# Optimization experiments

Hardware: AMD Instinct MI355X
Metric: run time of the kernel (lower is better)

## Reference

```python
import jax, jax.numpy as jnp
import numpy as np

OUT_H = 7  # _height_
OUT_W = 7  # _width_


def _bin_ids(start, end, size, nbins):
    # Per-pixel segment id along one spatial axis; id == nbins marks pixels outside the ROI.
    # Mirrors TF: step = int(region / nbins); bin i covers [i*step, (i+1)*step), last bin extends to region end.
    step = ((end - start).astype(jnp.float32) / nbins).astype(jnp.int32)
    idx = jnp.arange(size)
    rel = idx - start
    b = jnp.minimum(rel // jnp.maximum(step, 1), nbins - 1)
    b = jnp.where(step > 0, b, nbins - 1)  # degenerate step==0: everything valid falls in last bin
    valid = (rel >= 0) & (idx < end)
    return jnp.where(valid, b, nbins)


def _pool_one(fmap, roi):
    # fmap: [H, W, C], roi: [4] = (h_min, w_min, h_max, w_max) relative coords
    H, W, C = fmap.shape
    h0 = (H * roi[0]).astype(jnp.int32)
    w0 = (W * roi[1]).astype(jnp.int32)
    h1 = (H * roi[2]).astype(jnp.int32)
    w1 = (W * roi[3]).astype(jnp.int32)
    colb = _bin_ids(w0, w1, W, OUT_W)  # [W]
    rowb = _bin_ids(h0, h1, H, OUT_H)  # [H]
    # Max is separable over rows/cols: pool columns first, then rows.
    tmp = jax.ops.segment_max(jnp.transpose(fmap, (1, 0, 2)), colb, num_segments=OUT_W + 1)[:OUT_W]  # [OUT_W, H, C]
    out = jax.ops.segment_max(jnp.transpose(tmp, (1, 0, 2)), rowb, num_segments=OUT_H + 1)[:OUT_H]   # [OUT_H, OUT_W, C]
    return out


def _roi_pool(feature_map, rois):
    per_image = jax.vmap(_pool_one, in_axes=(None, 0))  # over ROIs
    return jax.vmap(per_image)(feature_map, rois)       # over batch -> [B, R, OUT_H, OUT_W, C]


def setup_inputs() -> dict:
    key = jax.random.key(0)
    k1, k2, k3 = jax.random.split(key, 3)
    B, H, W, C, R = 4, 56, 56, 256, 64
    feature_map = jax.random.normal(k1, (B, H, W, C), dtype=jnp.float32)
    # valid ROIs: (h_min, w_min) in [0, 0.45), extent in [0.30, 0.55) so every 7x7 bin is non-empty
    starts = jax.random.uniform(k2, (B, R, 2), minval=0.0, maxval=0.45, dtype=jnp.float32)
    lens = jax.random.uniform(k3, (B, R, 2), minval=0.30, maxval=0.55, dtype=jnp.float32)
    rois = jnp.concatenate([starts, jnp.minimum(starts + lens, 1.0)], axis=-1)  # [B, R, 4]
    return {"feature_map": feature_map, "rois": rois}


def reference(feature_map, rois):
    return _roi_pool(feature_map, rois)
```

## Files before the change

### kernel.cpp

```cpp
#include <hip/hip_runtime.h>


#define OUT_H 7
#define OUT_W 7
#define NBIN (OUT_H * OUT_W)
#define NB 4
#define NR 64
#define NH 56
#define NW 56
#define NC 256

#define BLKS_PER_XCD_SLOT 1568

typedef float v4f __attribute__((ext_vector_type(4)));

__global__ __launch_bounds__(64) void roi_pool_kernel(
    const float* __restrict__ fmap,
    const float* __restrict__ rois,
    float* __restrict__ out)
{
    const int blk  = blockIdx.x;
    const int xcd  = blk & 7;
    const int b    = xcd >> 1;
    const int work = ((xcd & 1) * BLKS_PER_XCD_SLOT) + (blk >> 3);
    const int r    = work / NBIN;
    const int bin  = work - r * NBIN;
    const int oi   = bin / OUT_W;
    const int oj   = bin - oi * OUT_W;

    const float* roi = rois + (size_t)(b * NR + r) * 4;
    const float r0 = roi[0], r1 = roi[1], r2 = roi[2], r3 = roi[3];
    const int h0 = (int)((float)NH * r0);
    const int w0 = (int)((float)NW * r1);
    const int h1 = (int)((float)NH * r2);
    const int w1 = (int)((float)NW * r3);

    const int hstep = (int)((float)(h1 - h0) / (float)OUT_H);
    const int wstep = (int)((float)(w1 - w0) / (float)OUT_W);

    int rlo, rhi, clo, chi;
    if (hstep >= 1) {
        rlo = h0 + oi * hstep;
        rhi = (oi < OUT_H - 1) ? (rlo + hstep) : h1;
    } else {
        rlo = (oi == OUT_H - 1) ? h0 : 0;
        rhi = (oi == OUT_H - 1) ? h1 : 0;
    }
    if (wstep >= 1) {
        clo = w0 + oj * wstep;
        chi = (oj < OUT_W - 1) ? (clo + wstep) : w1;
    } else {
        clo = (oj == OUT_W - 1) ? w0 : 0;
        chi = (oj == OUT_W - 1) ? w1 : 0;
    }

    const int tid = threadIdx.x;
    const int c4  = NC / 4;

    v4f acc = (v4f){-INFINITY, -INFINITY, -INFINITY, -INFINITY};

    for (int h = rlo; h < rhi; ++h) {
        const v4f* rowp =
            (const v4f*)(fmap + (size_t)(b * NH + h) * NW * NC);
        for (int w = clo; w < chi; ++w) {
            v4f v = rowp[(size_t)w * c4 + tid];
            acc.x = fmaxf(acc.x, v.x);
            acc.y = fmaxf(acc.y, v.y);
            acc.z = fmaxf(acc.z, v.z);
            acc.w = fmaxf(acc.w, v.w);
        }
    }

    const size_t obase = ((size_t)((b * NR + r) * NBIN + bin)) * NC;
    v4f* o = (v4f*)(out + obase);
    __builtin_nontemporal_store(acc, o + tid);
}

extern "C" void kernel_launch(void* const* d_in, const int* in_sizes, int n_in,
                              void* d_out, int out_size, void* d_ws, size_t ws_size,
                              hipStream_t stream) {
    const float* fmap = (const float*)d_in[0];
    const float* rois = (const float*)d_in[1];
    float* out = (float*)d_out;

    const int nblocks = NB * NR * NBIN;
    roi_pool_kernel<<<nblocks, 64, 0, stream>>>(fmap, rois, out);
}
```

Before: 19.63 us.

## Process a full output row of bins per block with templated column steps

Each block now computes all seven column bins of one output row instead of a single bin, so the grid shrinks from 12544 to 1792 blocks. Column pooling is specialised by templates for step sizes 2, 3 and 4, fully unrolling the inner loads so more independent loads are in flight per thread. This is meant to cut launch and scheduling overhead and the repeated ROI setup per bin. In exchange each block does more serial work, there is less parallelism across the GPU, and seven accumulators raise register use.

```diff
diff --git a/kernel.cpp b/kernel.cpp
--- a/kernel.cpp
+++ b/kernel.cpp
@@ -9,10 +9,45 @@
 #define NH 56
 #define NW 56
 #define NC 256
+#define C4 (NC / 4)
 
-#define BLKS_PER_XCD_SLOT 1568
+#define BLKS_PER_XCD_SLOT 224
 
 typedef float v4f __attribute__((ext_vector_type(4)));
+
+__device__ __forceinline__ v4f vmax4(v4f a, v4f b) {
+    v4f r;
+    r.x = fmaxf(a.x, b.x);
+    r.y = fmaxf(a.y, b.y);
+    r.z = fmaxf(a.z, b.z);
+    r.w = fmaxf(a.w, b.w);
+    return r;
+}
+
+template <int WS>
+__device__ __forceinline__ void pool_rows(
+    const v4f* __restrict__ base, int rlo, int rhi,
+    int w0, int w1, int wstep_rt, v4f* acc)
+{
+    const int ws = (WS > 0) ? WS : wstep_rt;
+    for (int h = rlo; h < rhi; ++h) {
+        const v4f* rowp = base + (size_t)(h * NW) * C4;
+#pragma unroll
+        for (int j = 0; j < OUT_W - 1; ++j) {
+            const int wb = w0 + j * ws;
+            if (WS > 0) {
+#pragma unroll
+                for (int k = 0; k < WS; ++k)
+                    acc[j] = vmax4(acc[j], rowp[(size_t)(wb + k) * C4]);
+            } else {
+                for (int w = wb; w < wb + ws; ++w)
+                    acc[j] = vmax4(acc[j], rowp[(size_t)w * C4]);
+            }
+        }
+        for (int w = w0 + 6 * ws; w < w1; ++w)
+            acc[6] = vmax4(acc[6], rowp[(size_t)w * C4]);
+    }
+}
 
 __global__ __launch_bounds__(64) void roi_pool_kernel(
     const float* __restrict__ fmap,
@@ -22,11 +57,11 @@
     const int blk  = blockIdx.x;
     const int xcd  = blk & 7;
     const int b    = xcd >> 1;
+    const int lane = threadIdx.x;
+
     const int work = ((xcd & 1) * BLKS_PER_XCD_SLOT) + (blk >> 3);
-    const int r    = work / NBIN;
-    const int bin  = work - r * NBIN;
-    const int oi   = bin / OUT_W;
-    const int oj   = bin - oi * OUT_W;
+    const int r    = work / OUT_H;
+    const int oi   = work - r * OUT_H;
 
     const float* roi = rois + (size_t)(b * NR + r) * 4;
     const float r0 = roi[0], r1 = roi[1], r2 = roi[2], r3 = roi[3];
@@ -38,7 +73,7 @@
     const int hstep = (int)((float)(h1 - h0) / (float)OUT_H);
     const int wstep = (int)((float)(w1 - w0) / (float)OUT_W);
 
-    int rlo, rhi, clo, chi;
+    int rlo, rhi;
     if (hstep >= 1) {
         rlo = h0 + oi * hstep;
         rhi = (oi < OUT_H - 1) ? (rlo + hstep) : h1;
@@ -46,34 +81,28 @@
         rlo = (oi == OUT_H - 1) ? h0 : 0;
         rhi = (oi == OUT_H - 1) ? h1 : 0;
     }
-    if (wstep >= 1) {
-        clo = w0 + oj * wstep;
-        chi = (oj < OUT_W - 1) ? (clo + wstep) : w1;
-    } else {
-        clo = (oj == OUT_W - 1) ? w0 : 0;
-        chi = (oj == OUT_W - 1) ? w1 : 0;
+
+    const v4f* base =
+        (const v4f*)(fmap + (size_t)b * NH * NW * NC) + lane;
+
+    const v4f ninf = (v4f){-INFINITY, -INFINITY, -INFINITY, -INFINITY};
+    v4f acc[OUT_W];
+#pragma unroll
+    for (int j = 0; j < OUT_W; ++j) acc[j] = ninf;
+
+    switch (wstep) {
+        case 2: pool_rows<2>(base, rlo, rhi, w0, w1, wstep, acc); break;
+        case 3: pool_rows<3>(base, rlo, rhi, w0, w1, wstep, acc); break;
+        case 4: pool_rows<4>(base, rlo, rhi, w0, w1, wstep, acc); break;
+        default: pool_rows<0>(base, rlo, rhi, w0, w1, wstep, acc); break;
     }
 
-    const int tid = threadIdx.x;
-    const int c4  = NC / 4;
-
-    v4f acc = (v4f){-INFINITY, -INFINITY, -INFINITY, -INFINITY};
-
-    for (int h = rlo; h < rhi; ++h) {
-        const v4f* rowp =
-            (const v4f*)(fmap + (size_t)(b * NH + h) * NW * NC);
-        for (int w = clo; w < chi; ++w) {
-            v4f v = rowp[(size_t)w * c4 + tid];
-            acc.x = fmaxf(acc.x, v.x);
-            acc.y = fmaxf(acc.y, v.y);
-            acc.z = fmaxf(acc.z, v.z);
-            acc.w = fmaxf(acc.w, v.w);
-        }
+    const size_t obase = ((size_t)((b * NR + r) * NBIN + oi * OUT_W)) * NC;
+#pragma unroll
+    for (int j = 0; j < OUT_W; ++j) {
+        v4f* o = (v4f*)(out + obase + (size_t)j * NC);
+        __builtin_nontemporal_store(acc[j], o + lane);
     }
-
-    const size_t obase = ((size_t)((b * NR + r) * NBIN + bin)) * NC;
-    v4f* o = (v4f*)(out + obase);
-    __builtin_nontemporal_store(acc, o + tid);
 }
 
 extern "C" void kernel_launch(void* const* d_in, const int* in_sizes, int n_in,
@@ -83,6 +112,6 @@
     const float* rois = (const float*)d_in[1];
     float* out = (float*)d_out;
 
-    const int nblocks = NB * NR * NBIN;
+    const int nblocks = NB * NR * OUT_H;
     roi_pool_kernel<<<nblocks, 64, 0, stream>>>(fmap, rois, out);
 }
```

Measured after the change: 22.02 us. +12.2%, slower.
